# Kernel optimization log

Hardware: AMD Instinct MI355X
Metric: run time of the kernel (lower is better)

Reference implementation:

```python
import jax, jax.numpy as jnp
import numpy as np

N_NODES = 100000
N_EDGES = 1600000
FEAT, HID, OUT = 256, 128, 64
N_BATCH = 10000
EPS = 1e-5


def gcn_conv(x, src, dst, W, b, n):
    # PyG GCNConv: linear -> add self loops -> sym-normalized scatter-add -> bias
    h = x @ W  # [N, C]
    loop = jnp.arange(n, dtype=src.dtype)
    s = jnp.concatenate([src, loop])
    d = jnp.concatenate([dst, loop])
    deg = jax.ops.segment_sum(jnp.ones_like(d, dtype=h.dtype), d, num_segments=n)
    dinv = jnp.where(deg > 0, jax.lax.rsqrt(deg), 0.0)
    norm = dinv[s] * dinv[d]                    # [E+N]
    msg = h[s] * norm[:, None]                  # gather + scale
    out = jax.ops.segment_sum(msg, d, num_segments=n)  # scatter-add
    return out + b


def batch_norm(x, gamma, beta):
    # training-mode BatchNorm1d: batch statistics, biased variance
    mu = jnp.mean(x, axis=0)
    var = jnp.var(x, axis=0)
    return (x - mu) * jax.lax.rsqrt(var + EPS) * gamma + beta


def setup_inputs() -> dict:
    key = jax.random.key(0)
    ks = jax.random.split(key, 8)
    features = jax.random.normal(ks[0], (N_NODES, FEAT), dtype=jnp.float32)
    edge_index = jax.random.randint(ks[1], (2, N_EDGES), 0, N_NODES, dtype=jnp.int64 if jax.config.jax_enable_x64 else jnp.int32)
    batch_nodes = jax.random.randint(ks[2], (N_BATCH,), 0, N_NODES, dtype=jnp.int32)
    W1 = jax.random.normal(ks[3], (FEAT, HID), dtype=jnp.float32) * (1.0 / np.sqrt(FEAT))
    b1 = jnp.zeros((HID,), jnp.float32)
    gamma1 = jnp.ones((HID,), jnp.float32)
    beta1 = jnp.zeros((HID,), jnp.float32)
    W2 = jax.random.normal(ks[4], (HID, OUT), dtype=jnp.float32) * (1.0 / np.sqrt(HID))
    b2 = jnp.zeros((OUT,), jnp.float32)
    gamma2 = jnp.ones((OUT,), jnp.float32)
    beta2 = jnp.zeros((OUT,), jnp.float32)
    return {"features": features, "edge_index": edge_index, "batch_nodes": batch_nodes,
            "W1": W1, "b1": b1, "gamma1": gamma1, "beta1": beta1,
            "W2": W2, "b2": b2, "gamma2": gamma2, "beta2": beta2}


def reference(features, edge_index, batch_nodes, W1, b1, gamma1, beta1, W2, b2, gamma2, beta2):
    src, dst = edge_index[0], edge_index[1]
    n = features.shape[0]
    x = gcn_conv(features, src, dst, W1, b1, n)
    x = jax.nn.relu(batch_norm(x, gamma1, beta1))
    # dropout treated as identity (deterministic reference)
    x = gcn_conv(x, src, dst, W2, b2, n)
    x = jax.nn.relu(batch_norm(x, gamma2, beta2))
    return jax.nn.log_softmax(x[batch_nodes], axis=1)
```

## Files before the change

kernel.cpp:

```cpp
#include <hip/hip_runtime.h>
#include <stdint.h>

typedef unsigned short bf16_t;

constexpr int kNN   = 100000;
constexpr int kNE   = 1600000;
constexpr int kFEAT = 256;
constexpr int kHID  = 128;
constexpr int kOUT  = 64;
constexpr int kNB   = 10000;
constexpr float kEPS = 1e-5f;

constexpr int kEPB  = 4096;
constexpr int kNBLK = (kNE + kEPB - 1) / kEPB;
constexpr int kNBUK = (kNN + 511) / 512;

typedef __attribute__((ext_vector_type(8))) short short8v;
typedef __attribute__((ext_vector_type(4))) float f32x4;

__device__ __forceinline__ float bf2f(bf16_t u) {
    union { uint32_t i; float f; } v; v.i = ((uint32_t)u) << 16; return v.f;
}
__device__ __forceinline__ bf16_t f2bf(float f) {
    uint32_t u = __float_as_uint(f);
    uint32_t r = (u + 0x7FFFu + ((u >> 16) & 1u)) >> 16;
    return (bf16_t)r;
}
__device__ __forceinline__ float lo16(uint32_t u) {
    union { uint32_t i; float f; } v; v.i = u << 16; return v.f;
}
__device__ __forceinline__ float hi16(uint32_t u) {
    union { uint32_t i; float f; } v; v.i = u & 0xFFFF0000u; return v.f;
}

#define ACC8(u) do { \
    acc[0] += lo16((u).x); acc[1] += hi16((u).x); \
    acc[2] += lo16((u).y); acc[3] += hi16((u).y); \
    acc[4] += lo16((u).z); acc[5] += hi16((u).z); \
    acc[6] += lo16((u).w); acc[7] += hi16((u).w); } while (0)

__global__ void k_probe(const uint32_t* __restrict__ feat, const uint32_t* __restrict__ ei,
                        int* __restrict__ flags) {
    int l = threadIdx.x;
    int good = 0;
    for (int j = l; j < 256; j += 64) {
        uint32_t e = (feat[j] >> 7) & 0xFFu;
        if (e >= 100u && e <= 132u) good++;
    }
    for (int o = 32; o; o >>= 1) good += __shfl_xor(good, o);
    int zeros = 0;
    for (int j = l; j < 128; j += 64) zeros += (ei[2 * j + 1] == 0u) ? 1 : 0;
    for (int o = 32; o; o >>= 1) zeros += __shfl_xor(zeros, o);
    if (l == 0) {
        flags[0] = (good > 128) ? 1 : 0;
        flags[1] = (zeros > 64) ? 1 : 0;
    }
}


__global__ void k_hist1(const int* __restrict__ ei, const int* __restrict__ flags,
                        unsigned int* __restrict__ counts) {
    __shared__ unsigned int lh[kNBUK];
    int t = threadIdx.x;
    for (int i = t; i < kNBUK; i += 256) lh[i] = 0u;
    __syncthreads();
    int i64 = flags[1];
    int base = blockIdx.x * kEPB;
    for (int k = 0; k < 16; k++) {
        int e = base + k * 256 + t;
        if (e < kNE) {
            int d = i64 ? ei[2 * (kNE + e)] : ei[kNE + e];
            atomicAdd(&lh[d >> 9], 1u);
        }
    }
    __syncthreads();
    for (int i = t; i < kNBUK; i += 256) counts[(size_t)i * kNBLK + blockIdx.x] = lh[i];
}

__global__ void k_scanA(const unsigned int* __restrict__ counts, unsigned int* __restrict__ base,
                        float* __restrict__ stats) {
    __shared__ unsigned int ss[256];
    int t = threadIdx.x;
    for (int i = t; i < 384; i += 256) stats[i] = 0.f;
    unsigned int tot = 0u;
    if (t < kNBUK) {
        const unsigned int* row = counts + (size_t)t * kNBLK;
        for (int j = 0; j < kNBLK; j++) tot += row[j];
    }
    ss[t] = tot;
    __syncthreads();
    for (int o = 1; o < 256; o <<= 1) {
        unsigned int x = (t >= o) ? ss[t - o] : 0u;
        __syncthreads();
        ss[t] += x;
        __syncthreads();
    }
    if (t < kNBUK) base[t] = ss[t] - tot;
    if (t == 0) base[kNBUK] = ss[255];
}

__global__ void k_scanB(const unsigned int* __restrict__ counts, const unsigned int* __restrict__ base,
                        unsigned int* __restrict__ off) {
    __shared__ unsigned int ss[64];
    int b = blockIdx.x, t = threadIdx.x;
    unsigned int run = base[b];
    for (int c0 = 0; c0 < kNBLK; c0 += 64) {
        int idx = c0 + t;
        unsigned int v = (idx < kNBLK) ? counts[(size_t)b * kNBLK + idx] : 0u;
        ss[t] = v;
        __syncthreads();
        for (int o = 1; o < 64; o <<= 1) {
            unsigned int x = (t >= o) ? ss[t - o] : 0u;
            __syncthreads();
            ss[t] += x;
            __syncthreads();
        }
        if (idx < kNBLK) off[(size_t)b * kNBLK + idx] = run + ss[t] - v;
        unsigned int ctot = ss[63];
        __syncthreads();
        run += ctot;
    }
}

__global__ void k_scatter1(const int* __restrict__ ei, const int* __restrict__ flags,
                           const unsigned int* __restrict__ off, unsigned int* __restrict__ pairs) {
    __shared__ unsigned int lcur[kNBUK];
    int t = threadIdx.x;
    for (int i = t; i < kNBUK; i += 256) lcur[i] = off[(size_t)i * kNBLK + blockIdx.x];
    __syncthreads();
    int i64 = flags[1];
    int base = blockIdx.x * kEPB;
    for (int k = 0; k < 16; k++) {
        int e = base + k * 256 + t;
        if (e < kNE) {
            int s, d;
            if (i64) { s = ei[2 * e]; d = ei[2 * (kNE + e)]; }
            else     { s = ei[e];     d = ei[kNE + e]; }
            unsigned int p = atomicAdd(&lcur[d >> 9], 1u);
            pairs[p] = (unsigned int)s | ((unsigned int)(d & 511) << 17);
        }
    }
}

__global__ void __launch_bounds__(1024) k_scatter2(const unsigned int* __restrict__ pairs,
                        const unsigned int* __restrict__ base, unsigned int* __restrict__ deg,
                        float* __restrict__ dinv, unsigned int* __restrict__ cursor,
                        int* __restrict__ sorted) {
    __shared__ unsigned int hist[512], sc[512], lcur[512];
    int b = blockIdx.x, t = threadIdx.x;
    unsigned int gb = base[b];
    int cnt = (int)(base[b + 1] - gb);
    if (t < 512) hist[t] = 0u;
    __syncthreads();
    for (int i = t; i < cnt; i += 1024) atomicAdd(&hist[pairs[gb + i] >> 17], 1u);
    __syncthreads();
    if (t < 512) sc[t] = hist[t];
    __syncthreads();
    for (int o = 1; o < 512; o <<= 1) {
        unsigned int x = 0u;
        if (t < 512 && t >= o) x = sc[t - o];
        __syncthreads();
        if (t < 512) sc[t] += x;
        __syncthreads();
    }
    if (t < 512) {
        lcur[t] = gb + sc[t] - hist[t];
        int node = b * 512 + t;
        if (node < kNN) {
            unsigned int dg = hist[t] + 1u;
            deg[node] = dg;
            dinv[node] = rsqrtf((float)dg);
            cursor[node] = gb + sc[t];
        }
    }
    __syncthreads();
    for (int i = t; i < cnt; i += 1024) {
        unsigned int pk = pairs[gb + i];
        unsigned int slot = atomicAdd(&lcur[pk >> 17], 1u);
        sorted[slot] = (int)(pk & 0x1FFFFu);
    }
}

__global__ void k_prepw(const void* __restrict__ W1, const void* __restrict__ W2,
                        const int* __restrict__ flags, bf16_t* __restrict__ Wz1,
                        bf16_t* __restrict__ Wz2) {
    int gid = blockIdx.x * 256 + threadIdx.x;
    int isbf = flags[0];
    if (gid < 4096) {
        int idx = gid;
        int l = idx & 63, j = (idx >> 6) & 7, t = idx >> 9;
        int col = j * 16 + (l & 15);
        int kb = t * 32 + (l >> 4) * 8;
        bf16_t o[8];
        if (isbf) {
            const bf16_t* Wb = (const bf16_t*)W1;
            #pragma unroll
            for (int i = 0; i < 8; i++) o[i] = Wb[(size_t)(kb + i) * kHID + col];
        } else {
            const float* Wf = (const float*)W1;
            #pragma unroll
            for (int i = 0; i < 8; i++) o[i] = f2bf(Wf[(size_t)(kb + i) * kHID + col]);
        }
        uint4 w;
        w.x = (uint32_t)o[0] | ((uint32_t)o[1] << 16);
        w.y = (uint32_t)o[2] | ((uint32_t)o[3] << 16);
        w.z = (uint32_t)o[4] | ((uint32_t)o[5] << 16);
        w.w = (uint32_t)o[6] | ((uint32_t)o[7] << 16);
        *(uint4*)(Wz1 + (size_t)idx * 8) = w;
    } else if (gid < 4096 + 1024) {
        int idx = gid - 4096;
        int l = idx & 63, j = (idx >> 6) & 3, t = idx >> 8;
        int col = j * 16 + (l & 15);
        int kb = t * 32 + (l >> 4) * 8;
        bf16_t o[8];
        if (isbf) {
            const bf16_t* Wb = (const bf16_t*)W2;
            #pragma unroll
            for (int i = 0; i < 8; i++) o[i] = Wb[(size_t)(kb + i) * kOUT + col];
        } else {
            const float* Wf = (const float*)W2;
            #pragma unroll
            for (int i = 0; i < 8; i++) o[i] = f2bf(Wf[(size_t)(kb + i) * kOUT + col]);
        }
        uint4 w;
        w.x = (uint32_t)o[0] | ((uint32_t)o[1] << 16);
        w.y = (uint32_t)o[2] | ((uint32_t)o[3] << 16);
        w.z = (uint32_t)o[4] | ((uint32_t)o[5] << 16);
        w.w = (uint32_t)o[6] | ((uint32_t)o[7] << 16);
        *(uint4*)(Wz2 + (size_t)idx * 8) = w;
    }
}

__global__ void k_gemm1(const void* __restrict__ A, const bf16_t* __restrict__ Wz,
                        const float* __restrict__ dinv, bf16_t* __restrict__ H,
                        const int* __restrict__ flags) {
    int isbf = flags[0];
    int wv = threadIdx.x >> 6;
    int l  = threadIdx.x & 63;
    int kgrp = l >> 4;
    int rbase = blockIdx.x * 128 + wv * 32;
    int arow0 = rbase + (l & 15);
    int arow1 = arow0 + 16;
    const bf16_t* Ab = (const bf16_t*)A;
    const float*  Af = (const float*)A;
    const short8v* Wv = (const short8v*)Wz;

    f32x4 acc[2][8];
    #pragma unroll
    for (int m = 0; m < 2; m++)
        #pragma unroll
        for (int j = 0; j < 8; j++)
            acc[m][j] = (f32x4){0.f, 0.f, 0.f, 0.f};

    #pragma unroll
    for (int t = 0; t < 8; t++) {
        int kbase = t * 32 + kgrp * 8;
        short8v a0, a1;
        #pragma unroll
        for (int i = 0; i < 8; i++) { a0[i] = 0; a1[i] = 0; }
        if (arow0 < kNN) {
            if (isbf) {
                a0 = *(const short8v*)(Ab + (size_t)arow0 * kFEAT + kbase);
            } else {
                const float* p = Af + (size_t)arow0 * kFEAT + kbase;
                #pragma unroll
                for (int i = 0; i < 8; i++) a0[i] = (short)f2bf(p[i]);
            }
        }
        if (arow1 < kNN) {
            if (isbf) {
                a1 = *(const short8v*)(Ab + (size_t)arow1 * kFEAT + kbase);
            } else {
                const float* p = Af + (size_t)arow1 * kFEAT + kbase;
                #pragma unroll
                for (int i = 0; i < 8; i++) a1[i] = (short)f2bf(p[i]);
            }
        }
        #pragma unroll
        for (int j = 0; j < 8; j++) {
            short8v b = Wv[(t * 8 + j) * 64 + l];
            acc[0][j] = __builtin_amdgcn_mfma_f32_16x16x32_bf16(a0, b, acc[0][j], 0, 0, 0);
            acc[1][j] = __builtin_amdgcn_mfma_f32_16x16x32_bf16(a1, b, acc[1][j], 0, 0, 0);
        }
    }

    #pragma unroll
    for (int m = 0; m < 2; m++) {
        #pragma unroll
        for (int r = 0; r < 4; r++) {
            int orow = rbase + m * 16 + kgrp * 4 + r;
            if (orow < kNN) {
                float dn = dinv[orow];
                bf16_t* hp = H + (size_t)orow * kHID + (l & 15);
                #pragma unroll
                for (int j = 0; j < 8; j++) hp[j * 16] = f2bf(acc[m][j][r] * dn);
            }
        }
    }
}

__global__ void k_agg1(const bf16_t* __restrict__ H, const int* __restrict__ sorted,
                       const unsigned int* __restrict__ cursor, const unsigned int* __restrict__ deg,
                       const float* __restrict__ dinv, const void* __restrict__ bias,
                       const int* __restrict__ flags, float* __restrict__ Out,
                       float* __restrict__ stats) {
    __shared__ float ss[256];
    int t = threadIdx.x;
    ss[t] = 0.f;
    __syncthreads();
    int g16 = t & 15;
    int grp = t >> 4;
    int c0 = g16 * 8;
    float bv[8];
    if (flags[0]) {
        const bf16_t* bb = (const bf16_t*)bias;
        #pragma unroll
        for (int j = 0; j < 8; j++) bv[j] = bf2f(bb[c0 + j]);
    } else {
        const float* bf = (const float*)bias;
        #pragma unroll
        for (int j = 0; j < 8; j++) bv[j] = bf[c0 + j];
    }
    for (int n0 = blockIdx.x * 16; n0 < kNN; n0 += gridDim.x * 16) {
        int n = n0 + grp;
        float acc[8];
        uint4 hs = *(const uint4*)(H + (size_t)n * kHID + c0);
        acc[0] = lo16(hs.x); acc[1] = hi16(hs.x);
        acc[2] = lo16(hs.y); acc[3] = hi16(hs.y);
        acc[4] = lo16(hs.z); acc[5] = hi16(hs.z);
        acc[6] = lo16(hs.w); acc[7] = hi16(hs.w);
        unsigned int e1 = cursor[n];
        int cnt = (int)(deg[n] - 1u);
        unsigned int e0 = e1 - (unsigned int)cnt;
        for (int base = 0; base < cnt; base += 16) {
            int idx = 0;
            if (base + g16 < cnt) idx = sorted[e0 + base + g16];
            int m = cnt - base; if (m > 16) m = 16;
            int j = 0;
            for (; j + 4 <= m; j += 4) {
                int s0 = __shfl(idx, j, 16);
                int s1 = __shfl(idx, j + 1, 16);
                int s2 = __shfl(idx, j + 2, 16);
                int s3 = __shfl(idx, j + 3, 16);
                uint4 u0 = *(const uint4*)(H + (size_t)s0 * kHID + c0);
                uint4 u1 = *(const uint4*)(H + (size_t)s1 * kHID + c0);
                uint4 u2 = *(const uint4*)(H + (size_t)s2 * kHID + c0);
                uint4 u3 = *(const uint4*)(H + (size_t)s3 * kHID + c0);
                ACC8(u0); ACC8(u1); ACC8(u2); ACC8(u3);
            }
            for (; j < m; j++) {
                int s = __shfl(idx, j, 16);
                uint4 u = *(const uint4*)(H + (size_t)s * kHID + c0);
                ACC8(u);
            }
        }
        float dn = dinv[n];
        float o[8];
        #pragma unroll
        for (int j = 0; j < 8; j++) o[j] = acc[j] * dn + bv[j];
        float4 w0 = {o[0], o[1], o[2], o[3]};
        float4 w1 = {o[4], o[5], o[6], o[7]};
        *(float4*)(Out + (size_t)n * kHID + c0) = w0;
        *(float4*)(Out + (size_t)n * kHID + c0 + 4) = w1;
        #pragma unroll
        for (int j = 0; j < 8; j++) {
            atomicAdd(&ss[c0 + j], o[j]);
            atomicAdd(&ss[128 + c0 + j], o[j] * o[j]);
        }
    }
    __syncthreads();
    atomicAdd(&stats[t], ss[t]);
}

__global__ void k_bnprep(const float* __restrict__ stats, const void* __restrict__ gamma,
                         const void* __restrict__ beta, const int* __restrict__ flags,
                         float* __restrict__ bnp) {
    int c = threadIdx.x;
    float mu = stats[c] * (1.f / kNN);
    float var = stats[128 + c] * (1.f / kNN) - mu * mu;
    float rs = rsqrtf(var + kEPS);
    float g, b;
    if (flags[0]) { g = bf2f(((const bf16_t*)gamma)[c]); b = bf2f(((const bf16_t*)beta)[c]); }
    else          { g = ((const float*)gamma)[c];        b = ((const float*)beta)[c]; }
    float sc = rs * g;
    bnp[c] = sc;
    bnp[128 + c] = b - mu * sc;
}

__global__ void k_gemm2(const float* A, const bf16_t* __restrict__ Wz,
                        const float* __restrict__ dinv, const float* __restrict__ bnp,
                        bf16_t* H ) {
    int wv = threadIdx.x >> 6;
    int l  = threadIdx.x & 63;
    int kgrp = l >> 4;
    int rbase = blockIdx.x * 128 + wv * 32;
    int arow0 = rbase + (l & 15);
    int arow1 = arow0 + 16;
    const short8v* Wv = (const short8v*)Wz;

    f32x4 acc[2][4];
    #pragma unroll
    for (int m = 0; m < 2; m++)
        #pragma unroll
        for (int j = 0; j < 4; j++)
            acc[m][j] = (f32x4){0.f, 0.f, 0.f, 0.f};

    #pragma unroll
    for (int t = 0; t < 4; t++) {
        int kbase = t * 32 + kgrp * 8;
        float4 sa = *(const float4*)(bnp + kbase);
        float4 sb = *(const float4*)(bnp + kbase + 4);
        float4 ha = *(const float4*)(bnp + 128 + kbase);
        float4 hb = *(const float4*)(bnp + 128 + kbase + 4);
        short8v a0, a1;
        #pragma unroll
        for (int i = 0; i < 8; i++) { a0[i] = 0; a1[i] = 0; }
        if (arow0 < kNN) {
            float4 f0 = *(const float4*)(A + (size_t)arow0 * kHID + kbase);
            float4 f1 = *(const float4*)(A + (size_t)arow0 * kHID + kbase + 4);
            float v;
            v = f0.x * sa.x + ha.x; a0[0] = (short)f2bf(v > 0.f ? v : 0.f);
            v = f0.y * sa.y + ha.y; a0[1] = (short)f2bf(v > 0.f ? v : 0.f);
            v = f0.z * sa.z + ha.z; a0[2] = (short)f2bf(v > 0.f ? v : 0.f);
            v = f0.w * sa.w + ha.w; a0[3] = (short)f2bf(v > 0.f ? v : 0.f);
            v = f1.x * sb.x + hb.x; a0[4] = (short)f2bf(v > 0.f ? v : 0.f);
            v = f1.y * sb.y + hb.y; a0[5] = (short)f2bf(v > 0.f ? v : 0.f);
            v = f1.z * sb.z + hb.z; a0[6] = (short)f2bf(v > 0.f ? v : 0.f);
            v = f1.w * sb.w + hb.w; a0[7] = (short)f2bf(v > 0.f ? v : 0.f);
        }
        if (arow1 < kNN) {
            float4 f0 = *(const float4*)(A + (size_t)arow1 * kHID + kbase);
            float4 f1 = *(const float4*)(A + (size_t)arow1 * kHID + kbase + 4);
            float v;
            v = f0.x * sa.x + ha.x; a1[0] = (short)f2bf(v > 0.f ? v : 0.f);
            v = f0.y * sa.y + ha.y; a1[1] = (short)f2bf(v > 0.f ? v : 0.f);
            v = f0.z * sa.z + ha.z; a1[2] = (short)f2bf(v > 0.f ? v : 0.f);
            v = f0.w * sa.w + ha.w; a1[3] = (short)f2bf(v > 0.f ? v : 0.f);
            v = f1.x * sb.x + hb.x; a1[4] = (short)f2bf(v > 0.f ? v : 0.f);
            v = f1.y * sb.y + hb.y; a1[5] = (short)f2bf(v > 0.f ? v : 0.f);
            v = f1.z * sb.z + hb.z; a1[6] = (short)f2bf(v > 0.f ? v : 0.f);
            v = f1.w * sb.w + hb.w; a1[7] = (short)f2bf(v > 0.f ? v : 0.f);
        }
        #pragma unroll
        for (int j = 0; j < 4; j++) {
            short8v b = Wv[(t * 4 + j) * 64 + l];
            acc[0][j] = __builtin_amdgcn_mfma_f32_16x16x32_bf16(a0, b, acc[0][j], 0, 0, 0);
            acc[1][j] = __builtin_amdgcn_mfma_f32_16x16x32_bf16(a1, b, acc[1][j], 0, 0, 0);
        }
    }

    #pragma unroll
    for (int m = 0; m < 2; m++) {
        #pragma unroll
        for (int r = 0; r < 4; r++) {
            int orow = rbase + m * 16 + kgrp * 4 + r;
            if (orow < kNN) {
                float dn = dinv[orow];
                bf16_t* hp = H + (size_t)orow * 256 + (l & 15);
                #pragma unroll
                for (int j = 0; j < 4; j++) hp[j * 16] = f2bf(acc[m][j][r] * dn);
            }
        }
    }
}

__global__ void k_agg2(const bf16_t* __restrict__ H, const int* __restrict__ sorted,
                       const unsigned int* __restrict__ cursor, const unsigned int* __restrict__ deg,
                       const float* __restrict__ dinv, const void* __restrict__ bias,
                       const int* __restrict__ flags, float* __restrict__ Out,
                       float* __restrict__ stats) {
    __shared__ float ss[128];
    int t = threadIdx.x;
    if (t < 128) ss[t] = 0.f;
    __syncthreads();
    int g8 = t & 7;
    int grp = t >> 3;
    int c0 = g8 * 8;
    float bv[8];
    if (flags[0]) {
        const bf16_t* bb = (const bf16_t*)bias;
        #pragma unroll
        for (int j = 0; j < 8; j++) bv[j] = bf2f(bb[c0 + j]);
    } else {
        const float* bf = (const float*)bias;
        #pragma unroll
        for (int j = 0; j < 8; j++) bv[j] = bf[c0 + j];
    }
    for (int n0 = blockIdx.x * 32; n0 < kNN; n0 += gridDim.x * 32) {
        int n = n0 + grp;
        float acc[8];
        uint4 hs = *(const uint4*)(H + (size_t)n * 256 + c0);
        acc[0] = lo16(hs.x); acc[1] = hi16(hs.x);
        acc[2] = lo16(hs.y); acc[3] = hi16(hs.y);
        acc[4] = lo16(hs.z); acc[5] = hi16(hs.z);
        acc[6] = lo16(hs.w); acc[7] = hi16(hs.w);
        unsigned int e1 = cursor[n];
        int cnt = (int)(deg[n] - 1u);
        unsigned int e0 = e1 - (unsigned int)cnt;
        for (int base = 0; base < cnt; base += 8) {
            int idx = 0;
            if (base + g8 < cnt) idx = sorted[e0 + base + g8];
            int m = cnt - base; if (m > 8) m = 8;
            int j = 0;
            for (; j + 4 <= m; j += 4) {
                int s0 = __shfl(idx, j, 8);
                int s1 = __shfl(idx, j + 1, 8);
                int s2 = __shfl(idx, j + 2, 8);
                int s3 = __shfl(idx, j + 3, 8);
                uint4 u0 = *(const uint4*)(H + (size_t)s0 * 256 + c0);
                uint4 u1 = *(const uint4*)(H + (size_t)s1 * 256 + c0);
                uint4 u2 = *(const uint4*)(H + (size_t)s2 * 256 + c0);
                uint4 u3 = *(const uint4*)(H + (size_t)s3 * 256 + c0);
                ACC8(u0); ACC8(u1); ACC8(u2); ACC8(u3);
            }
            for (; j < m; j++) {
                int s = __shfl(idx, j, 8);
                uint4 u = *(const uint4*)(H + (size_t)s * 256 + c0);
                ACC8(u);
            }
        }
        float dn = dinv[n];
        float o[8];
        #pragma unroll
        for (int j = 0; j < 8; j++) o[j] = acc[j] * dn + bv[j];
        float4 w0 = {o[0], o[1], o[2], o[3]};
        float4 w1 = {o[4], o[5], o[6], o[7]};
        *(float4*)(Out + (size_t)n * kOUT + c0) = w0;
        *(float4*)(Out + (size_t)n * kOUT + c0 + 4) = w1;
        #pragma unroll
        for (int j = 0; j < 8; j++) {
            atomicAdd(&ss[c0 + j], o[j]);
            atomicAdd(&ss[64 + c0 + j], o[j] * o[j]);
        }
    }
    __syncthreads();
    if (t < 64)  atomicAdd(&stats[256 + t], ss[t]);
    else if (t < 128) atomicAdd(&stats[320 + (t - 64)], ss[t]);
}

__global__ void k_out(const float* __restrict__ A2, const float* __restrict__ stats,
                      const int* __restrict__ batch, const void* __restrict__ gamma,
                      const void* __restrict__ beta, const int* __restrict__ flags,
                      bf16_t* __restrict__ out) {
    int wid = threadIdx.x >> 6;
    int lane = threadIdx.x & 63;
    int i = blockIdx.x * 4 + wid;
    if (i >= kNB) return;
    int n = batch[i];
    int c = lane;
    float mu = stats[256 + c] * (1.f / kNN);
    float var = stats[320 + c] * (1.f / kNN) - mu * mu;
    float g, b;
    if (flags[0]) { g = bf2f(((const bf16_t*)gamma)[c]); b = bf2f(((const bf16_t*)beta)[c]); }
    else          { g = ((const float*)gamma)[c];        b = ((const float*)beta)[c]; }
    float v = (A2[(size_t)n * kOUT + c] - mu) * rsqrtf(var + kEPS) * g + b;
    v = v > 0.f ? v : 0.f;
    float m = v;
    for (int o = 32; o; o >>= 1) m = fmaxf(m, __shfl_xor(m, o));
    float ex = expf(v - m);
    float s = ex;
    for (int o = 32; o; o >>= 1) s += __shfl_xor(s, o);
    float r = v - m - logf(s);
    if (flags[0]) out[(size_t)i * kOUT + c] = f2bf(r);
    else ((float*)out)[(size_t)i * kOUT + c] = r;
}

static inline size_t align_up(size_t x, size_t a) { return (x + a - 1) & ~(a - 1); }

extern "C" void kernel_launch(void* const* d_in, const int* in_sizes, int n_in,
                              void* d_out, int out_size, void* d_ws, size_t ws_size,
                              hipStream_t stream) {
    (void)in_sizes; (void)n_in; (void)out_size; (void)ws_size;
    const void* feat = d_in[0];
    const int* ei    = (const int*)d_in[1];
    const int* batch = (const int*)d_in[2];
    const void* W1   = d_in[3];
    const void* b1   = d_in[4];
    const void* g1   = d_in[5];
    const void* be1  = d_in[6];
    const void* W2   = d_in[7];
    const void* b2   = d_in[8];
    const void* g2   = d_in[9];
    const void* be2  = d_in[10];

    char* ws = (char*)d_ws;
    size_t o = 0;
    int*          flags  = (int*)(ws + o);          o = align_up(o + 32, 256);
    unsigned int* deg    = (unsigned int*)(ws + o); o = align_up(o + (size_t)kNN * 4, 256);
    float*        dinv   = (float*)(ws + o);        o = align_up(o + (size_t)kNN * 4, 256);
    unsigned int* cursor = (unsigned int*)(ws + o); o = align_up(o + (size_t)kNN * 4, 256);
    float*        stats  = (float*)(ws + o);        o = align_up(o + 384 * 4, 256);
    float*        bnp    = (float*)(ws + o);        o = align_up(o + 256 * 4, 256);
    int*          sorted = (int*)(ws + o);          o = align_up(o + (size_t)kNE * 4, 256);
    bf16_t*       h1     = (bf16_t*)(ws + o);       o = align_up(o + (size_t)kNN * kHID * 2, 256);
    float*        a1     = (float*)(ws + o);        o = align_up(o + (size_t)kNN * kHID * 4, 256);
    bf16_t*       wz1    = (bf16_t*)(ws + o);       o = align_up(o + (size_t)8 * 8 * 64 * 8 * 2, 256);
    bf16_t*       wz2    = (bf16_t*)(ws + o);       o = align_up(o + (size_t)4 * 4 * 64 * 8 * 2, 256);

    unsigned int* pairs  = (unsigned int*)h1;
    unsigned int* counts = (unsigned int*)a1;
    unsigned int* offm   = (unsigned int*)((char*)a1 + 512 * 1024);
    unsigned int* gbase  = (unsigned int*)((char*)a1 + 1024 * 1024);

    bf16_t*       h2 = (bf16_t*)a1;
    float*        a2 = (float*)h1;

    bf16_t* outp = (bf16_t*)d_out;

    k_probe   <<<1, 64, 0, stream>>>((const uint32_t*)feat, (const uint32_t*)ei, flags);
    k_prepw   <<<20, 256, 0, stream>>>(W1, W2, flags, wz1, wz2);
    k_hist1   <<<kNBLK, 256, 0, stream>>>(ei, flags, counts);
    k_scanA   <<<1, 256, 0, stream>>>(counts, gbase, stats);
    k_scanB   <<<kNBUK, 64, 0, stream>>>(counts, gbase, offm);
    k_scatter1<<<kNBLK, 256, 0, stream>>>(ei, flags, offm, pairs);
    k_scatter2<<<kNBUK, 1024, 0, stream>>>(pairs, gbase, deg, dinv, cursor, sorted);

    k_gemm1 <<<(kNN + 127) / 128, 256, 0, stream>>>(feat, wz1, dinv, h1, flags);
    k_agg1  <<<2048, 256, 0, stream>>>(h1, sorted, cursor, deg, dinv, b1, flags, a1, stats);
    k_bnprep<<<1, 128, 0, stream>>>(stats, g1, be1, flags, bnp);

    k_gemm2<<<(kNN + 127) / 128, 256, 0, stream>>>(a1, wz2, dinv, bnp, h2);
    k_agg2 <<<1024, 256, 0, stream>>>(h2, sorted, cursor, deg, dinv, b2, flags, a2, stats);

    k_out<<<(kNB + 3) / 4, 256, 0, stream>>>(a2, stats, batch, g2, be2, flags, outp);
}
```

Before: 537.1 us.

## Remap GCN aggregation to one wavefront per node with register-held BN stats

Both aggregation kernels now give each node a full wavefront (layer 1) or a 32-lane half (layer 2). Each lane gathers one 32-bit word holding two bf16 channels, eight neighbour rows at a time. Neighbour indices are read directly as group-uniform loads instead of being broadcast by shuffles. BatchNorm sum and sum-of-squares are kept in registers across all nodes a thread handles and flushed to shared memory once, replacing per-node shared-memory atomics. The trade is narrower per-lane loads (4 bytes instead of 16) and more rows in flight per group, which changes memory-level parallelism and coalescing behaviour.

Result: faster. 477.8 us (-11.0%).

```diff
diff --git a/kernel.cpp b/kernel.cpp
--- a/kernel.cpp
+++ b/kernel.cpp
@@ -32,12 +32,6 @@
 __device__ __forceinline__ float hi16(uint32_t u) {
     union { uint32_t i; float f; } v; v.i = u & 0xFFFF0000u; return v.f;
 }
-
-#define ACC8(u) do { \
-    acc[0] += lo16((u).x); acc[1] += hi16((u).x); \
-    acc[2] += lo16((u).y); acc[3] += hi16((u).y); \
-    acc[4] += lo16((u).z); acc[5] += hi16((u).z); \
-    acc[6] += lo16((u).w); acc[7] += hi16((u).w); } while (0)
 
 __global__ void k_probe(const uint32_t* __restrict__ feat, const uint32_t* __restrict__ ei,
                         int* __restrict__ flags) {
@@ -307,67 +301,53 @@
     __shared__ float ss[256];
     int t = threadIdx.x;
     ss[t] = 0.f;
-    __syncthreads();
-    int g16 = t & 15;
-    int grp = t >> 4;
-    int c0 = g16 * 8;
-    float bv[8];
-    if (flags[0]) {
-        const bf16_t* bb = (const bf16_t*)bias;
-        #pragma unroll
-        for (int j = 0; j < 8; j++) bv[j] = bf2f(bb[c0 + j]);
-    } else {
-        const float* bf = (const float*)bias;
-        #pragma unroll
-        for (int j = 0; j < 8; j++) bv[j] = bf[c0 + j];
-    }
-    for (int n0 = blockIdx.x * 16; n0 < kNN; n0 += gridDim.x * 16) {
-        int n = n0 + grp;
-        float acc[8];
-        uint4 hs = *(const uint4*)(H + (size_t)n * kHID + c0);
-        acc[0] = lo16(hs.x); acc[1] = hi16(hs.x);
-        acc[2] = lo16(hs.y); acc[3] = hi16(hs.y);
-        acc[4] = lo16(hs.z); acc[5] = hi16(hs.z);
-        acc[6] = lo16(hs.w); acc[7] = hi16(hs.w);
+    int wv = t >> 6;
+    int lane = t & 63;
+    int c0 = lane * 2;
+    float b0, b1v;
+    if (flags[0]) { b0 = bf2f(((const bf16_t*)bias)[c0]); b1v = bf2f(((const bf16_t*)bias)[c0 + 1]); }
+    else          { b0 = ((const float*)bias)[c0];        b1v = ((const float*)bias)[c0 + 1]; }
+    const uint32_t* Hrow = (const uint32_t*)H;
+    float ps0 = 0.f, ps1 = 0.f, pq0 = 0.f, pq1 = 0.f;
+    for (int n = blockIdx.x * 4 + wv; n < kNN; n += gridDim.x * 4) {
+        float dn = dinv[n];
+        uint32_t hu = Hrow[(size_t)n * 64 + lane];
+        float acc0 = lo16(hu), acc1 = hi16(hu);
         unsigned int e1 = cursor[n];
         int cnt = (int)(deg[n] - 1u);
-        unsigned int e0 = e1 - (unsigned int)cnt;
-        for (int base = 0; base < cnt; base += 16) {
-            int idx = 0;
-            if (base + g16 < cnt) idx = sorted[e0 + base + g16];
-            int m = cnt - base; if (m > 16) m = 16;
-            int j = 0;
-            for (; j + 4 <= m; j += 4) {
-                int s0 = __shfl(idx, j, 16);
-                int s1 = __shfl(idx, j + 1, 16);
-                int s2 = __shfl(idx, j + 2, 16);
-                int s3 = __shfl(idx, j + 3, 16);
-                uint4 u0 = *(const uint4*)(H + (size_t)s0 * kHID + c0);
-                uint4 u1 = *(const uint4*)(H + (size_t)s1 * kHID + c0);
-                uint4 u2 = *(const uint4*)(H + (size_t)s2 * kHID + c0);
-                uint4 u3 = *(const uint4*)(H + (size_t)s3 * kHID + c0);
-                ACC8(u0); ACC8(u1); ACC8(u2); ACC8(u3);
-            }
-            for (; j < m; j++) {
-                int s = __shfl(idx, j, 16);
-                uint4 u = *(const uint4*)(H + (size_t)s * kHID + c0);
-                ACC8(u);
-            }
-        }
-        float dn = dinv[n];
-        float o[8];
-        #pragma unroll
-        for (int j = 0; j < 8; j++) o[j] = acc[j] * dn + bv[j];
-        float4 w0 = {o[0], o[1], o[2], o[3]};
-        float4 w1 = {o[4], o[5], o[6], o[7]};
-        *(float4*)(Out + (size_t)n * kHID + c0) = w0;
-        *(float4*)(Out + (size_t)n * kHID + c0 + 4) = w1;
-        #pragma unroll
-        for (int j = 0; j < 8; j++) {
-            atomicAdd(&ss[c0 + j], o[j]);
-            atomicAdd(&ss[128 + c0 + j], o[j] * o[j]);
-        }
-    }
+        unsigned int e = e1 - (unsigned int)cnt;
+        for (; cnt >= 8; cnt -= 8, e += 8) {
+            int s0 = sorted[e],     s1 = sorted[e + 1], s2 = sorted[e + 2], s3 = sorted[e + 3];
+            int s4 = sorted[e + 4], s5 = sorted[e + 5], s6 = sorted[e + 6], s7 = sorted[e + 7];
+            uint32_t u0 = Hrow[(size_t)s0 * 64 + lane];
+            uint32_t u1 = Hrow[(size_t)s1 * 64 + lane];
+            uint32_t u2 = Hrow[(size_t)s2 * 64 + lane];
+            uint32_t u3 = Hrow[(size_t)s3 * 64 + lane];
+            uint32_t u4 = Hrow[(size_t)s4 * 64 + lane];
+            uint32_t u5 = Hrow[(size_t)s5 * 64 + lane];
+            uint32_t u6 = Hrow[(size_t)s6 * 64 + lane];
+            uint32_t u7 = Hrow[(size_t)s7 * 64 + lane];
+            acc0 += lo16(u0) + lo16(u1) + lo16(u2) + lo16(u3)
+                  + lo16(u4) + lo16(u5) + lo16(u6) + lo16(u7);
+            acc1 += hi16(u0) + hi16(u1) + hi16(u2) + hi16(u3)
+                  + hi16(u4) + hi16(u5) + hi16(u6) + hi16(u7);
+        }
+        for (; cnt > 0; cnt--, e++) {
+            uint32_t u = Hrow[(size_t)sorted[e] * 64 + lane];
+            acc0 += lo16(u);
+            acc1 += hi16(u);
+        }
+        float ox = acc0 * dn + b0;
+        float oy = acc1 * dn + b1v;
+        float2 o; o.x = ox; o.y = oy;
+        *(float2*)(Out + (size_t)n * kHID + c0) = o;
+        ps0 += ox; ps1 += oy; pq0 += ox * ox; pq1 += oy * oy;
+    }
+    __syncthreads();
+    atomicAdd(&ss[c0], ps0);
+    atomicAdd(&ss[c0 + 1], ps1);
+    atomicAdd(&ss[128 + c0], pq0);
+    atomicAdd(&ss[128 + c0 + 1], pq1);
     __syncthreads();
     atomicAdd(&stats[t], ss[t]);
 }
@@ -472,67 +452,53 @@
     __shared__ float ss[128];
     int t = threadIdx.x;
     if (t < 128) ss[t] = 0.f;
-    __syncthreads();
-    int g8 = t & 7;
-    int grp = t >> 3;
-    int c0 = g8 * 8;
-    float bv[8];
-    if (flags[0]) {
-        const bf16_t* bb = (const bf16_t*)bias;
-        #pragma unroll
-        for (int j = 0; j < 8; j++) bv[j] = bf2f(bb[c0 + j]);
-    } else {
-        const float* bf = (const float*)bias;
-        #pragma unroll
-        for (int j = 0; j < 8; j++) bv[j] = bf[c0 + j];
-    }
-    for (int n0 = blockIdx.x * 32; n0 < kNN; n0 += gridDim.x * 32) {
-        int n = n0 + grp;
-        float acc[8];
-        uint4 hs = *(const uint4*)(H + (size_t)n * 256 + c0);
-        acc[0] = lo16(hs.x); acc[1] = hi16(hs.x);
-        acc[2] = lo16(hs.y); acc[3] = hi16(hs.y);
-        acc[4] = lo16(hs.z); acc[5] = hi16(hs.z);
-        acc[6] = lo16(hs.w); acc[7] = hi16(hs.w);
+    int grp = t >> 5;
+    int lane = t & 31;
+    int c0 = lane * 2;
+    float b0, b1v;
+    if (flags[0]) { b0 = bf2f(((const bf16_t*)bias)[c0]); b1v = bf2f(((const bf16_t*)bias)[c0 + 1]); }
+    else          { b0 = ((const float*)bias)[c0];        b1v = ((const float*)bias)[c0 + 1]; }
+    const uint32_t* Hrow = (const uint32_t*)H;
+    float ps0 = 0.f, ps1 = 0.f, pq0 = 0.f, pq1 = 0.f;
+    for (int n = blockIdx.x * 8 + grp; n < kNN; n += gridDim.x * 8) {
+        float dn = dinv[n];
+        uint32_t hu = Hrow[(size_t)n * 128 + lane];
+        float acc0 = lo16(hu), acc1 = hi16(hu);
         unsigned int e1 = cursor[n];
         int cnt = (int)(deg[n] - 1u);
-        unsigned int e0 = e1 - (unsigned int)cnt;
-        for (int base = 0; base < cnt; base += 8) {
-            int idx = 0;
-            if (base + g8 < cnt) idx = sorted[e0 + base + g8];
-            int m = cnt - base; if (m > 8) m = 8;
-            int j = 0;
-            for (; j + 4 <= m; j += 4) {
-                int s0 = __shfl(idx, j, 8);
-                int s1 = __shfl(idx, j + 1, 8);
-                int s2 = __shfl(idx, j + 2, 8);
-                int s3 = __shfl(idx, j + 3, 8);
-                uint4 u0 = *(const uint4*)(H + (size_t)s0 * 256 + c0);
-                uint4 u1 = *(const uint4*)(H + (size_t)s1 * 256 + c0);
-                uint4 u2 = *(const uint4*)(H + (size_t)s2 * 256 + c0);
-                uint4 u3 = *(const uint4*)(H + (size_t)s3 * 256 + c0);
-                ACC8(u0); ACC8(u1); ACC8(u2); ACC8(u3);
-            }
-            for (; j < m; j++) {
-                int s = __shfl(idx, j, 8);
-                uint4 u = *(const uint4*)(H + (size_t)s * 256 + c0);
-                ACC8(u);
-            }
-        }
-        float dn = dinv[n];
-        float o[8];
-        #pragma unroll
-        for (int j = 0; j < 8; j++) o[j] = acc[j] * dn + bv[j];
-        float4 w0 = {o[0], o[1], o[2], o[3]};
-        float4 w1 = {o[4], o[5], o[6], o[7]};
-        *(float4*)(Out + (size_t)n * kOUT + c0) = w0;
-        *(float4*)(Out + (size_t)n * kOUT + c0 + 4) = w1;
-        #pragma unroll
-        for (int j = 0; j < 8; j++) {
-            atomicAdd(&ss[c0 + j], o[j]);
-            atomicAdd(&ss[64 + c0 + j], o[j] * o[j]);
-        }
-    }
+        unsigned int e = e1 - (unsigned int)cnt;
+        for (; cnt >= 8; cnt -= 8, e += 8) {
+            int s0 = sorted[e],     s1 = sorted[e + 1], s2 = sorted[e + 2], s3 = sorted[e + 3];
+            int s4 = sorted[e + 4], s5 = sorted[e + 5], s6 = sorted[e + 6], s7 = sorted[e + 7];
+            uint32_t u0 = Hrow[(size_t)s0 * 128 + lane];
+            uint32_t u1 = Hrow[(size_t)s1 * 128 + lane];
+            uint32_t u2 = Hrow[(size_t)s2 * 128 + lane];
+            uint32_t u3 = Hrow[(size_t)s3 * 128 + lane];
+            uint32_t u4 = Hrow[(size_t)s4 * 128 + lane];
+            uint32_t u5 = Hrow[(size_t)s5 * 128 + lane];
+            uint32_t u6 = Hrow[(size_t)s6 * 128 + lane];
+            uint32_t u7 = Hrow[(size_t)s7 * 128 + lane];
+            acc0 += lo16(u0) + lo16(u1) + lo16(u2) + lo16(u3)
+                  + lo16(u4) + lo16(u5) + lo16(u6) + lo16(u7);
+            acc1 += hi16(u0) + hi16(u1) + hi16(u2) + hi16(u3)
+                  + hi16(u4) + hi16(u5) + hi16(u6) + hi16(u7);
+        }
+        for (; cnt > 0; cnt--, e++) {
+            uint32_t u = Hrow[(size_t)sorted[e] * 128 + lane];
+            acc0 += lo16(u);
+            acc1 += hi16(u);
+        }
+        float ox = acc0 * dn + b0;
+        float oy = acc1 * dn + b1v;
+        float2 o; o.x = ox; o.y = oy;
+        *(float2*)(Out + (size_t)n * kOUT + c0) = o;
+        ps0 += ox; ps1 += oy; pq0 += ox * ox; pq1 += oy * oy;
+    }
+    __syncthreads();
+    atomicAdd(&ss[c0], ps0);
+    atomicAdd(&ss[c0 + 1], ps1);
+    atomicAdd(&ss[64 + c0], pq0);
+    atomicAdd(&ss[64 + c0 + 1], pq1);
     __syncthreads();
     if (t < 64)  atomicAdd(&stats[256 + t], ss[t]);
     else if (t < 128) atomicAdd(&stats[320 + (t - 64)], ss[t]);
```
